# Performance work log

Hardware: AMD Instinct MI355X
Metric: run time of the kernel (lower is better)

Reference implementation:

```python
import jax, jax.numpy as jnp
import numpy as np

NEG_INF = -1e9  # matches masked_fill value in the torch source


def setup_inputs() -> dict:
    key0 = jax.random.key(0)
    kq, kk, kv, km = jax.random.split(key0, 4)
    B, H, S, D = 2, 12, 2048, 64
    query = jax.random.normal(kq, (B, H, S, D), dtype=jnp.float32)
    key = jax.random.normal(kk, (B, H, S, D), dtype=jnp.float32)
    value = jax.random.normal(kv, (B, H, S, D), dtype=jnp.float32)
    mask = jax.random.randint(km, (B, S, S), 0, 2, dtype=jnp.int32)
    return {"query": query, "key": key, "value": value, "mask": mask}


def reference(query, key, value, mask):
    # query/key/value: [B, H, S, D]; mask: [B, S, S] (0 = masked out)
    d = key.shape[-1]
    scale = 1.0 / np.sqrt(d).astype(np.float32)
    # attn scores: [B, H, Sq, Sk]
    attn = jnp.einsum("bhqd,bhkd->bhqk", query * scale, key)
    m = mask[:, None, :, :]  # broadcast over heads, mirrors mask.unsqueeze(1)
    attn = jnp.where(m == 0, jnp.float32(NEG_INF), attn)
    attn = jax.nn.softmax(attn, axis=-1)
    # dropout_ratio = 0.0 -> identity
    out = jnp.einsum("bhqk,bhkd->bhqd", attn, value)
    return out
```

## Files before the change

### kernel.cpp

```cpp
#include <hip/hip_runtime.h>

#define SQ 2048
#define DH 64
#define NH 12
#define NBH 24

typedef __attribute__((ext_vector_type(8))) short short8;
typedef __attribute__((ext_vector_type(16))) float f32x16;

union U8 { uint4 u; short8 s; };

__device__ __forceinline__ unsigned short f2bf(float x) {
  union { float f; unsigned u; } v; v.f = x;
  return (unsigned short)((v.u + 0x7FFFu + ((v.u >> 16) & 1u)) >> 16);
}

__device__ __forceinline__ unsigned pk2(float a, float b) {
  unsigned ua = __builtin_bit_cast(unsigned, a) + 0x8000u;
  unsigned ub = __builtin_bit_cast(unsigned, b) + 0x8000u;
  return __builtin_amdgcn_perm(ub, ua, 0x07060302);
}

__device__ __forceinline__ float bflo(unsigned w) {
  return __builtin_bit_cast(float, w << 16);
}
__device__ __forceinline__ float bfhi(unsigned w) {
  return __builtin_bit_cast(float, w & 0xFFFF0000u);
}

__device__ __forceinline__ void gload_lds16(const void* g, void* l) {
  __builtin_amdgcn_global_load_lds(
      (const __attribute__((address_space(1))) unsigned*)g,
      (__attribute__((address_space(3))) unsigned*)l, 16, 0, 0);
}

__device__ __forceinline__ int sw23(int x) {
  return (x & 19) | ((x & 4) << 1) | ((x & 8) >> 1);
}

__global__ __launch_bounds__(256) void prep_all(
    const float* __restrict__ Q, const float* __restrict__ K,
    const float* __restrict__ V, const int* __restrict__ M,
    unsigned short* __restrict__ Qb, unsigned short* __restrict__ Kb,
    unsigned short* __restrict__ Vt, unsigned* __restrict__ mbits) {
  const int bid = blockIdx.x, tid = threadIdx.x;
  if (bid < 3072) {
    int i = bid * 256 + tid;
    float4 q = ((const float4*)Q)[i];
    float4 k = ((const float4*)K)[i];
    const float sc = 0.125f * 1.44269504f;
    ushort4 qo, ko;
    qo.x = f2bf(q.x * sc); qo.y = f2bf(q.y * sc);
    qo.z = f2bf(q.z * sc); qo.w = f2bf(q.w * sc);
    ko.x = f2bf(k.x); ko.y = f2bf(k.y); ko.z = f2bf(k.z); ko.w = f2bf(k.w);
    ((ushort4*)Qb)[i] = qo;
    ((ushort4*)Kb)[i] = ko;
  } else if (bid < 3840) {
    __shared__ float T[64 * 65];
    int bx = bid - 3072;
    int bh = bx >> 5, st = bx & 31;
    int s0 = st * 64;
    int c4 = (tid & 15) * 4, r0 = tid >> 4;
#pragma unroll
    for (int it = 0; it < 4; ++it) {
      int r = r0 + 16 * it;
      float4 v = *(const float4*)(V + ((size_t)(bh * SQ + s0 + r)) * DH + c4);
      T[r * 65 + c4 + 0] = v.x; T[r * 65 + c4 + 1] = v.y;
      T[r * 65 + c4 + 2] = v.z; T[r * 65 + c4 + 3] = v.w;
    }
    __syncthreads();
#pragma unroll
    for (int it = 0; it < 2; ++it) {
      int cc = tid + 256 * it;
      int d = cc >> 3, c8 = (cc & 7) * 8;
      short8 o;
#pragma unroll
      for (int j = 0; j < 8; ++j) o[j] = (short)f2bf(T[(c8 + j) * 65 + d]);
      *(short8*)(Vt + ((size_t)(bh * 64 + d)) * SQ + s0 + c8) = o;
    }
  } else {
    int w = tid >> 6, lane = tid & 63;
    int row = (bid - 3840) * 4 + w;
    const int* mrow = M + (size_t)row * SQ;
    unsigned long long out = 0;
#pragma unroll
    for (int j = 0; j < 32; ++j) {
      int mv = mrow[j * 64 + lane];
      unsigned long long bits = __ballot(mv != 0);
      if (lane == j) out = bits;
    }
    if (lane < 32)
      ((unsigned long long*)mbits)[(size_t)row * 32 + lane] = out;
  }
}

__global__ __launch_bounds__(256, 3) void attn_kernel(
    const unsigned short* __restrict__ Qb, const unsigned short* __restrict__ Kb,
    const unsigned short* __restrict__ Vt, const unsigned* __restrict__ mbits,
    unsigned short* __restrict__ Ob, float* __restrict__ Lp) {
  __shared__ uint4 FIFO[2][16][64];

  const int bx = blockIdx.x;
  const int bh = bx % NBH;
  const int rest = bx / NBH;
  const int qt = rest & 15, ks = rest >> 4;
  const int b = bh / NH;
  const int tid = threadIdx.x;
  const int lane = tid & 63, w = tid >> 6;
  const int n = lane & 31, h = lane >> 5;
  const int qrow = qt * 128 + w * 32 + n;
  const int k0 = ks * (SQ / 2);

  short8 qf[4];
#pragma unroll
  for (int s = 0; s < 4; ++s)
    qf[s] = *(const short8*)(Qb + ((size_t)(bh * SQ + qrow)) * DH + 16 * s + 8 * h);

  const unsigned short* gp[4];
  if (w < 2) {
#pragma unroll
    for (int j = 0; j < 4; ++j) {
      int c = 4 * w + j;
      int row = k0 + 32 * (c >> 2) + sw23(n);
      gp[j] = Kb + ((size_t)bh * SQ + row) * DH + 16 * (c & 3) + 8 * h;
    }
  } else {
#pragma unroll
    for (int j = 0; j < 4; ++j) {
      int cc = 4 * (w - 2) + j;
      gp[j] = Vt + ((size_t)bh * DH + 32 * (cc >> 2) + n) * SQ + k0 + 16 * (cc & 3) + 8 * h;
    }
  }
  const int gstride = (w < 2) ? 64 * DH : 64;
  const int chunk0 = w * 4;

  const unsigned long long* mp =
      (const unsigned long long*)mbits + ((size_t)b * SQ + qrow) * 32 + (k0 >> 6);

  short8 ones;
#pragma unroll
  for (int j = 0; j < 8; ++j) ones[j] = (short)0x3F80;

  f32x16 acc0 = {0,0,0,0,0,0,0,0,0,0,0,0,0,0,0,0};
  f32x16 acc1 = {0,0,0,0,0,0,0,0,0,0,0,0,0,0,0,0};
  f32x16 sumac = {0,0,0,0,0,0,0,0,0,0,0,0,0,0,0,0};

#pragma unroll
  for (int j = 0; j < 4; ++j) {
    gload_lds16(gp[j], &FIFO[0][chunk0 + j][0]);
    gp[j] += gstride;
  }
  __syncthreads();

  for (int nt = 0; nt < 16; ++nt) {
    const int cur = nt & 1;
    if (nt < 15) {
#pragma unroll
      for (int j = 0; j < 4; ++j) {
        gload_lds16(gp[j], &FIFO[1 - cur][chunk0 + j][0]);
        gp[j] += gstride;
      }
    }
    unsigned long long mg = *mp; ++mp;

    short8 pb[2][2];
#pragma unroll
    for (int u = 0; u < 2; ++u) {
      f32x16 st = {0,0,0,0,0,0,0,0,0,0,0,0,0,0,0,0};
#pragma unroll
      for (int s = 0; s < 4; ++s) {
        U8 kf; kf.u = FIFO[cur][4 * u + s][lane];
        st = __builtin_amdgcn_mfma_f32_32x32x16_bf16(kf.s, qf[s], st, 0, 0, 0);
      }
      unsigned blo = (unsigned)(mg >> (8 * (4 * u + h))) & 0xFFu;
      unsigned bhi = (unsigned)(mg >> (8 * (4 * u + 2 + h))) & 0xFFu;
      float p[16];
#pragma unroll
      for (int j = 0; j < 16; ++j) {
        float e = __builtin_amdgcn_exp2f(st[j]);
        unsigned byt = (j < 8) ? blo : bhi;
        p[j] = ((byt >> (j & 7)) & 1u) ? e : 0.f;
      }
      U8 x0, x1;
      x0.u = (uint4){pk2(p[0], p[1]), pk2(p[2], p[3]), pk2(p[4], p[5]), pk2(p[6], p[7])};
      x1.u = (uint4){pk2(p[8], p[9]), pk2(p[10], p[11]), pk2(p[12], p[13]), pk2(p[14], p[15])};
      pb[u][0] = x0.s;
      pb[u][1] = x1.s;
    }

#pragma unroll
    for (int t = 0; t < 4; ++t) {
      short8 pf = pb[t >> 1][t & 1];
      sumac = __builtin_amdgcn_mfma_f32_32x32x16_bf16(ones, pf, sumac, 0, 0, 0);
      U8 v0; v0.u = FIFO[cur][8 + t][lane];
      acc0 = __builtin_amdgcn_mfma_f32_32x32x16_bf16(v0.s, pf, acc0, 0, 0, 0);
      U8 v1; v1.u = FIFO[cur][12 + t][lane];
      acc1 = __builtin_amdgcn_mfma_f32_32x32x16_bf16(v1.s, pf, acc1, 0, 0, 0);
    }

    __syncthreads();
  }

  unsigned short* rb = Ob + 128 * (size_t)(bh * SQ + qrow) + 64 * ks;
#pragma unroll
  for (int dt = 0; dt < 2; ++dt) {
    f32x16 A = dt ? acc1 : acc0;
#pragma unroll
    for (int a = 0; a < 4; ++a) {
      uint2 o = {pk2(A[4 * a], A[4 * a + 1]), pk2(A[4 * a + 2], A[4 * a + 3])};
      *(uint2*)(rb + 32 * dt + 8 * a + 4 * h) = o;
    }
  }
  if (lane < 32) Lp[(size_t)ks * NBH * SQ + bh * SQ + qrow] = sumac[0];
}

__global__ __launch_bounds__(256) void combine(float* __restrict__ Out,
                                               const float* __restrict__ Lp) {
  int i = blockIdx.x * 256 + threadIdx.x;
  int r = i >> 4;
  int d0 = (i & 15) * 4;
  const unsigned short* ob = (const unsigned short*)Out;
  uint2 p0 = *(const uint2*)(ob + 128 * (size_t)r + d0);
  uint2 p1 = *(const uint2*)(ob + 128 * (size_t)r + 64 + d0);
  float inv = __builtin_amdgcn_rcpf(Lp[r] + Lp[NBH * SQ + r]);
  float4 o = {(bflo(p0.x) + bflo(p1.x)) * inv, (bfhi(p0.x) + bfhi(p1.x)) * inv,
              (bflo(p0.y) + bflo(p1.y)) * inv, (bfhi(p0.y) + bfhi(p1.y)) * inv};
  ((float4*)Out)[i] = o;
}

extern "C" void kernel_launch(void* const* d_in, const int* in_sizes, int n_in,
                              void* d_out, int out_size, void* d_ws, size_t ws_size,
                              hipStream_t stream) {
  const float* Q = (const float*)d_in[0];
  const float* K = (const float*)d_in[1];
  const float* V = (const float*)d_in[2];
  const int*   M = (const int*)d_in[3];
  float* Out = (float*)d_out;

  size_t NB = (size_t)NBH * SQ * DH;
  unsigned short* Qb = (unsigned short*)d_ws;
  unsigned short* Kb = Qb + NB;
  unsigned short* Vt = Kb + NB;
  unsigned* mbits = (unsigned*)(Vt + NB);
  float* Lp = (float*)(mbits + (size_t)2 * SQ * 64);

  prep_all<<<4864, 256, 0, stream>>>(Q, K, V, M, Qb, Kb, Vt, mbits);
  attn_kernel<<<NBH * 16 * 2, 256, 0, stream>>>(Qb, Kb, Vt, mbits,
                                                (unsigned short*)Out, Lp);
  combine<<<(int)(NB / 4 / 256), 256, 0, stream>>>(Out, Lp);
}
```

Measured before the change: 155.0 us.

## Load K/V fragments directly from global into registers, dropping LDS double-buffer

Removes the shared-memory FIFO, the global_load_lds double buffering and the per-tile barrier. Each wave now loads its own K and V^T MFMA fragments straight from global memory into registers and splits the score computation into two halves so the loads can overlap compute. This drops LDS traffic and block-wide synchronisation, but all four waves redundantly fetch the same K/V tiles, which raises global/L2 traffic and register pressure and leaves no explicit prefetch across iterations.

```diff
diff --git a/kernel.cpp b/kernel.cpp
--- a/kernel.cpp
+++ b/kernel.cpp
@@ -26,12 +26,6 @@
 }
 __device__ __forceinline__ float bfhi(unsigned w) {
   return __builtin_bit_cast(float, w & 0xFFFF0000u);
-}
-
-__device__ __forceinline__ void gload_lds16(const void* g, void* l) {
-  __builtin_amdgcn_global_load_lds(
-      (const __attribute__((address_space(1))) unsigned*)g,
-      (__attribute__((address_space(3))) unsigned*)l, 16, 0, 0);
 }
 
 __device__ __forceinline__ int sw23(int x) {
@@ -98,8 +92,6 @@
     const unsigned short* __restrict__ Qb, const unsigned short* __restrict__ Kb,
     const unsigned short* __restrict__ Vt, const unsigned* __restrict__ mbits,
     unsigned short* __restrict__ Ob, float* __restrict__ Lp) {
-  __shared__ uint4 FIFO[2][16][64];
-
   const int bx = blockIdx.x;
   const int bh = bx % NBH;
   const int rest = bx / NBH;
@@ -116,23 +108,14 @@
   for (int s = 0; s < 4; ++s)
     qf[s] = *(const short8*)(Qb + ((size_t)(bh * SQ + qrow)) * DH + 16 * s + 8 * h);
 
-  const unsigned short* gp[4];
-  if (w < 2) {
-#pragma unroll
-    for (int j = 0; j < 4; ++j) {
-      int c = 4 * w + j;
-      int row = k0 + 32 * (c >> 2) + sw23(n);
-      gp[j] = Kb + ((size_t)bh * SQ + row) * DH + 16 * (c & 3) + 8 * h;
-    }
-  } else {
-#pragma unroll
-    for (int j = 0; j < 4; ++j) {
-      int cc = 4 * (w - 2) + j;
-      gp[j] = Vt + ((size_t)bh * DH + 32 * (cc >> 2) + n) * SQ + k0 + 16 * (cc & 3) + 8 * h;
-    }
-  }
-  const int gstride = (w < 2) ? 64 * DH : 64;
-  const int chunk0 = w * 4;
+  const unsigned short* kp[2];
+#pragma unroll
+  for (int u = 0; u < 2; ++u)
+    kp[u] = Kb + ((size_t)bh * SQ + k0 + 32 * u + sw23(n)) * DH + 8 * h;
+  const unsigned short* vp[2];
+#pragma unroll
+  for (int dt = 0; dt < 2; ++dt)
+    vp[dt] = Vt + ((size_t)bh * DH + 32 * dt + n) * SQ + k0 + 8 * h;
 
   const unsigned long long* mp =
       (const unsigned long long*)mbits + ((size_t)b * SQ + qrow) * 32 + (k0 >> 6);
@@ -145,60 +128,73 @@
   f32x16 acc1 = {0,0,0,0,0,0,0,0,0,0,0,0,0,0,0,0};
   f32x16 sumac = {0,0,0,0,0,0,0,0,0,0,0,0,0,0,0,0};
 
-#pragma unroll
-  for (int j = 0; j < 4; ++j) {
-    gload_lds16(gp[j], &FIFO[0][chunk0 + j][0]);
-    gp[j] += gstride;
-  }
-  __syncthreads();
-
   for (int nt = 0; nt < 16; ++nt) {
-    const int cur = nt & 1;
-    if (nt < 15) {
-#pragma unroll
-      for (int j = 0; j < 4; ++j) {
-        gload_lds16(gp[j], &FIFO[1 - cur][chunk0 + j][0]);
-        gp[j] += gstride;
-      }
-    }
     unsigned long long mg = *mp; ++mp;
 
+    U8 kf0[4], kf1[4];
+#pragma unroll
+    for (int s = 0; s < 4; ++s) kf0[s].u = *(const uint4*)(kp[0] + 16 * s);
+#pragma unroll
+    for (int s = 0; s < 4; ++s) kf1[s].u = *(const uint4*)(kp[1] + 16 * s);
+
+    f32x16 st0 = {0,0,0,0,0,0,0,0,0,0,0,0,0,0,0,0};
+#pragma unroll
+    for (int s = 0; s < 4; ++s)
+      st0 = __builtin_amdgcn_mfma_f32_32x32x16_bf16(kf0[s].s, qf[s], st0, 0, 0, 0);
+
+    U8 vf0[4], vf1[4];
+#pragma unroll
+    for (int t = 0; t < 4; ++t) vf0[t].u = *(const uint4*)(vp[0] + 16 * t);
+#pragma unroll
+    for (int t = 0; t < 4; ++t) vf1[t].u = *(const uint4*)(vp[1] + 16 * t);
+
     short8 pb[2][2];
-#pragma unroll
-    for (int u = 0; u < 2; ++u) {
-      f32x16 st = {0,0,0,0,0,0,0,0,0,0,0,0,0,0,0,0};
-#pragma unroll
-      for (int s = 0; s < 4; ++s) {
-        U8 kf; kf.u = FIFO[cur][4 * u + s][lane];
-        st = __builtin_amdgcn_mfma_f32_32x32x16_bf16(kf.s, qf[s], st, 0, 0, 0);
-      }
-      unsigned blo = (unsigned)(mg >> (8 * (4 * u + h))) & 0xFFu;
-      unsigned bhi = (unsigned)(mg >> (8 * (4 * u + 2 + h))) & 0xFFu;
+    {
+      unsigned blo = (unsigned)(mg >> (8 * (0 + h))) & 0xFFu;
+      unsigned bhi = (unsigned)(mg >> (8 * (2 + h))) & 0xFFu;
       float p[16];
 #pragma unroll
       for (int j = 0; j < 16; ++j) {
-        float e = __builtin_amdgcn_exp2f(st[j]);
+        float e = __builtin_amdgcn_exp2f(st0[j]);
         unsigned byt = (j < 8) ? blo : bhi;
         p[j] = ((byt >> (j & 7)) & 1u) ? e : 0.f;
       }
       U8 x0, x1;
       x0.u = (uint4){pk2(p[0], p[1]), pk2(p[2], p[3]), pk2(p[4], p[5]), pk2(p[6], p[7])};
       x1.u = (uint4){pk2(p[8], p[9]), pk2(p[10], p[11]), pk2(p[12], p[13]), pk2(p[14], p[15])};
-      pb[u][0] = x0.s;
-      pb[u][1] = x1.s;
+      pb[0][0] = x0.s; pb[0][1] = x1.s;
+    }
+
+    f32x16 st1 = {0,0,0,0,0,0,0,0,0,0,0,0,0,0,0,0};
+#pragma unroll
+    for (int s = 0; s < 4; ++s)
+      st1 = __builtin_amdgcn_mfma_f32_32x32x16_bf16(kf1[s].s, qf[s], st1, 0, 0, 0);
+    {
+      unsigned blo = (unsigned)(mg >> (8 * (4 + h))) & 0xFFu;
+      unsigned bhi = (unsigned)(mg >> (8 * (6 + h))) & 0xFFu;
+      float p[16];
+#pragma unroll
+      for (int j = 0; j < 16; ++j) {
+        float e = __builtin_amdgcn_exp2f(st1[j]);
+        unsigned byt = (j < 8) ? blo : bhi;
+        p[j] = ((byt >> (j & 7)) & 1u) ? e : 0.f;
+      }
+      U8 x0, x1;
+      x0.u = (uint4){pk2(p[0], p[1]), pk2(p[2], p[3]), pk2(p[4], p[5]), pk2(p[6], p[7])};
+      x1.u = (uint4){pk2(p[8], p[9]), pk2(p[10], p[11]), pk2(p[12], p[13]), pk2(p[14], p[15])};
+      pb[1][0] = x0.s; pb[1][1] = x1.s;
     }
 
 #pragma unroll
     for (int t = 0; t < 4; ++t) {
       short8 pf = pb[t >> 1][t & 1];
       sumac = __builtin_amdgcn_mfma_f32_32x32x16_bf16(ones, pf, sumac, 0, 0, 0);
-      U8 v0; v0.u = FIFO[cur][8 + t][lane];
-      acc0 = __builtin_amdgcn_mfma_f32_32x32x16_bf16(v0.s, pf, acc0, 0, 0, 0);
-      U8 v1; v1.u = FIFO[cur][12 + t][lane];
-      acc1 = __builtin_amdgcn_mfma_f32_32x32x16_bf16(v1.s, pf, acc1, 0, 0, 0);
-    }
-
-    __syncthreads();
+      acc0 = __builtin_amdgcn_mfma_f32_32x32x16_bf16(vf0[t].s, pf, acc0, 0, 0, 0);
+      acc1 = __builtin_amdgcn_mfma_f32_32x32x16_bf16(vf1[t].s, pf, acc1, 0, 0, 0);
+    }
+
+    kp[0] += 64 * DH; kp[1] += 64 * DH;
+    vp[0] += 64;      vp[1] += 64;
   }
 
   unsigned short* rb = Ob + 128 * (size_t)(bh * SQ + qrow) + 64 * ks;
```

Result: slower. 207.5 us (+33.9%).
